# Performance work log

Measured on AMD Instinct MI355X. Metric: run time of the kernel, lower is better.

## Reference

```python
import jax, jax.numpy as jnp
import numpy as np

B, I, C, J, D, H, W = 16, 32, 8, 10, 16, 6, 6
NUM_ROUTING = 3
EPS = 1e-07


def setup_inputs() -> dict:
    key = jax.random.key(0)
    u_hat = jax.random.normal(key, (B, I, C, J, D, H, W), dtype=jnp.float32)
    # torch module fills bias with 0.1, shape (out_capsules, out_channels, 1, 1)
    bias = jnp.full((J, D, 1, 1), 0.1, dtype=jnp.float32)
    return {"u_hat": u_hat, "bias": bias, "num_routing": NUM_ROUTING}


def _squash(s):
    # Faithful to the source: L1 norm over ALL non-batch dims (not per-capsule L2).
    n1 = jnp.sum(jnp.abs(s), axis=(1, 2, 3, 4), keepdims=True)  # [B,1,1,1,1]
    n1_sq = n1 * n1
    return (n1_sq / (1.0 + n1_sq)) * (s / (n1 + EPS))


def reference(u_hat, bias, num_routing):
    # u_hat: [B,I,C,J,D,H,W]; bias: [J,D,1,1]
    b_ij = jnp.zeros((I, J), dtype=u_hat.dtype)
    v_j = None
    for _ in range(num_routing):
        c_ij = jax.nn.softmax(b_ij, axis=1)  # [I,J]
        # s_j[b,j,d,h,w] = sum_{i,c} c[i,j] * u_hat[b,i,c,j,d,h,w]  (c broadcast over in_channels)
        s_j = jnp.einsum('ij,bicjdhw->bjdhw', c_ij, u_hat) + bias
        v_j = _squash(s_j)  # [B,J,D,H,W]
        # agreement[i,j] = sum over b,c,d,h,w of u_hat * v_j (broadcast over i,c)
        agreement = jnp.einsum('bicjdhw,bjdhw->ij', u_hat, v_j)
        b_ij = b_ij + jax.lax.stop_gradient(agreement)  # torch uses .data (detached)
    return v_j
```

## Files before the change

kernel.cpp:

```cpp
#include <hip/hip_runtime.h>


#define NB   16
#define NI   32
#define NC   8
#define NJ   10
#define ND   16
#define NHW  36
#define NDHW 576
#define CK   3
#define CHK  192
#define NBJ  (NB * NJ)
#define NBJC (NBJ * CK)
#define NJDHW (NJ * NDHW)
#define NTOT  (NB * NJ * NDHW)
#define EPSV 1e-7f
#define TPB  192

static __device__ __forceinline__ double wave_sum(double v) {
    #pragma unroll
    for (int off = 32; off > 0; off >>= 1) v += __shfl_down(v, off);
    return v;
}

static __device__ __forceinline__ void n1_reduce(float sv, double* slot,
                                                 double* nred ) {
    int tid = threadIdx.x;
    double a = wave_sum((double)fabsf(sv));
    if ((tid & 63) == 0) nred[tid >> 6] = a;
    __syncthreads();
    if (tid == 0) slot[0] = (nred[0] + nred[1]) + nred[2];
}

static __device__ __forceinline__ void g_reduce(const float* Uv, float sv,
                                                double* gslot,
                                                double (*gred)[32] ) {
    int tid = threadIdx.x, w = tid >> 6, lane = tid & 63;
    #pragma unroll
    for (int i = 0; i < NI; ++i) {
        double p = wave_sum((double)Uv[i] * (double)sv);
        if (lane == 0) gred[w][i] = p;
    }
    __syncthreads();
    if (tid < NI)
        gslot[tid] = (gred[0][tid] + gred[1][tid]) + gred[2][tid];
}

__global__ __launch_bounds__(TPB) void a1_kernel(
    const float4* __restrict__ uh4, const float* __restrict__ bias,
    float4* __restrict__ U2f4, double* __restrict__ n1p, double* __restrict__ Gp)
{
    __shared__ float4  Utile4[NI * 48];
    __shared__ double  nred[3];
    __shared__ double  gred[3][32];

    const int blk = blockIdx.x;
    const int bj = blk / CK, ck = blk - bj * CK;
    const int b = bj / NJ,  j  = bj - b * NJ;
    const int tid = threadIdx.x;

    #pragma unroll
    for (int g = 0; g < 8; ++g) {
        int lin = g * TPB + tid;
        int i  = lin / 48, f4 = lin - i * 48;
        const float4* p = uh4 + ((size_t)(b * NI + i) * NC) * 1440
                              + j * 144 + ck * 48 + f4;
        float4 acc = make_float4(0.f, 0.f, 0.f, 0.f);
        #pragma unroll
        for (int c = 0; c < NC; ++c) {
            float4 v = p[(size_t)c * 1440];
            acc.x += v.x; acc.y += v.y; acc.z += v.z; acc.w += v.w;
        }
        Utile4[lin] = acc;
        U2f4[(size_t)bj * 4608 + i * 144 + ck * 48 + f4] = acc;
    }
    __syncthreads();

    const float* Utile = (const float*)Utile4;
    const float cw = 1.0f / 10.0f;
    float Uv[NI];
    float sv = bias[j * ND + (ck * CHK + tid) / NHW];
    #pragma unroll
    for (int i = 0; i < NI; ++i) {
        Uv[i] = Utile[i * CHK + tid];
        sv += cw * Uv[i];
    }

    n1_reduce(sv, &n1p[blk], nred);
    g_reduce(Uv, sv, &Gp[(size_t)blk * NI], gred);
}

template <int R>
__global__ __launch_bounds__(TPB) void ab_kernel(
    const float* __restrict__ U2, const float* __restrict__ bias,
    const double* __restrict__ n1p, double* __restrict__ Gp,
    double* __restrict__ n1p_out, double* __restrict__ Gp_out,
    float* __restrict__ s)
{
    __shared__ double sc_sh[2][NB];
    __shared__ float  bij_sh[NI * NJ];
    __shared__ float  c_sh[NI];
    __shared__ double nred[3];
    __shared__ double gred[3][32];

    const int blk = blockIdx.x;
    const int bj = blk / CK, ck = blk - bj * CK;
    const int b = bj / NJ,  j  = bj - b * NJ;
    const int tid = threadIdx.x;

    if (tid < R * NB) {
        int rr = tid / NB, bb = tid - rr * NB;
        double n1 = 0.0;
        #pragma unroll
        for (int jj = 0; jj < NJ; ++jj)
            #pragma unroll
            for (int cc = 0; cc < CK; ++cc)
                n1 += n1p[(size_t)rr * NBJC + (bb * NJ + jj) * CK + cc];
        double nsq = n1 * n1;
        sc_sh[rr][bb] = (nsq / (1.0 + nsq)) / (n1 + (double)EPSV);
    }
    __syncthreads();

    for (int e = tid; e < NI * NJ; e += TPB) {
        int i = e / NJ, jj = e - i * NJ;
        double a = 0.0;
        for (int rr = 0; rr < R; ++rr)
            #pragma unroll
            for (int bb = 0; bb < NB; ++bb)
                #pragma unroll
                for (int cc = 0; cc < CK; ++cc)
                    a += sc_sh[rr][bb] *
                         Gp[(size_t)rr * (NBJC * NI) +
                            (size_t)((bb * NJ + jj) * CK + cc) * NI + i];
        bij_sh[e] = (float)a;
    }
    __syncthreads();

    if (tid < NI) {
        float m = -1e30f;
        #pragma unroll
        for (int jj = 0; jj < NJ; ++jj) m = fmaxf(m, bij_sh[tid * NJ + jj]);
        float sum = 0.f;
        #pragma unroll
        for (int jj = 0; jj < NJ; ++jj) sum += expf(bij_sh[tid * NJ + jj] - m);
        c_sh[tid] = expf(bij_sh[tid * NJ + j] - m) / sum;
    }
    __syncthreads();

    const float* u2b = U2 + (size_t)bj * 18432 + ck * CHK + tid;
    float Uv[NI];
    float sv = bias[j * ND + (ck * CHK + tid) / NHW];
    #pragma unroll
    for (int i = 0; i < NI; ++i) {
        Uv[i] = u2b[i * NDHW];
        sv += c_sh[i] * Uv[i];
    }

    if (R == 2) s[(size_t)bj * NDHW + ck * CHK + tid] = sv;

    n1_reduce(sv, &n1p_out[blk], nred);
    if (R == 1)
        g_reduce(Uv, sv, &Gp_out[(size_t)blk * NI], gred);
}

__global__ __launch_bounds__(256) void v_kernel(
    const float* __restrict__ s, const double* __restrict__ n1p2,
    float* __restrict__ out)
{
    int e = blockIdx.x * 256 + threadIdx.x;
    int b = e / NJDHW;
    double n1 = 0.0;
    #pragma unroll
    for (int jj = 0; jj < NJ; ++jj)
        #pragma unroll
        for (int cc = 0; cc < CK; ++cc)
            n1 += n1p2[(b * NJ + jj) * CK + cc];
    float n1f = (float)n1;
    float nsq = n1f * n1f;
    out[e] = (nsq / (1.f + nsq)) * (s[e] / (n1f + EPSV));
}

extern "C" void kernel_launch(void* const* d_in, const int* in_sizes, int n_in,
                              void* d_out, int out_size, void* d_ws, size_t ws_size,
                              hipStream_t stream)
{
    const float* u_hat = (const float*)d_in[0];
    const float* bias  = (const float*)d_in[1];

    float*  U2  = (float*)d_ws;
    float*  s   = U2 + (size_t)NB * NJ * NI * NDHW;
    double* n1p = (double*)(s + NTOT);
    double* Gp  = n1p + 3 * NBJC;
    float*  out = (float*)d_out;

    a1_kernel<<<NBJC, TPB, 0, stream>>>(
        (const float4*)u_hat, bias, (float4*)U2, n1p, Gp);
    ab_kernel<1><<<NBJC, TPB, 0, stream>>>(
        U2, bias, n1p, Gp, n1p + NBJC, Gp + NBJC * NI, s);
    ab_kernel<2><<<NBJC, TPB, 0, stream>>>(
        U2, bias, n1p, Gp, n1p + 2 * NBJC, nullptr, s);
    v_kernel<<<NTOT / 256, 256, 0, stream>>>(s, n1p + 2 * NBJC, out);
}
```

Before: 209.3 us.

## Fuse final routing iteration and squash into per-batch kernel, transpose Gp layout

Replaces the second routing kernel and the separate squash kernel with one per-batch kernel. It computes all coupling coefficients, builds s in shared memory, reduces the L1 norm in-block and writes the output directly. This removes one launch and the global round trip of s. The partial-agreement buffer is also reordered so the b_ij reductions read contiguous memory. The trade-off is that the final kernel runs only 16 large blocks, which may underuse the GPU while streaming U2.

```diff
diff --git a/kernel.cpp b/kernel.cpp
--- a/kernel.cpp
+++ b/kernel.cpp
@@ -12,10 +12,15 @@
 #define CHK  192
 #define NBJ  (NB * NJ)
 #define NBJC (NBJ * CK)
-#define NJDHW (NJ * NDHW)
 #define NTOT  (NB * NJ * NDHW)
 #define EPSV 1e-7f
 #define TPB  192
+#define FTPB 1024
+#define GP_ITER (NJ * NI * NB * CK)
+#define GP_J    (NI * NB * CK)
+#define GP_I    (NB * CK)
+#define N1_ITER (NB * NJ * CK)
+#define N1_B    (NJ * CK)
 
 static __device__ __forceinline__ double wave_sum(double v) {
     #pragma unroll
@@ -32,9 +37,9 @@
     if (tid == 0) slot[0] = (nred[0] + nred[1]) + nred[2];
 }
 
-static __device__ __forceinline__ void g_reduce(const float* Uv, float sv,
-                                                double* gslot,
-                                                double (*gred)[32] ) {
+static __device__ __forceinline__ void g_reduce_t(const float* Uv, float sv,
+                                                  double* gbase,
+                                                  double (*gred)[32] ) {
     int tid = threadIdx.x, w = tid >> 6, lane = tid & 63;
     #pragma unroll
     for (int i = 0; i < NI; ++i) {
@@ -43,7 +48,7 @@
     }
     __syncthreads();
     if (tid < NI)
-        gslot[tid] = (gred[0][tid] + gred[1][tid]) + gred[2][tid];
+        gbase[tid * GP_I] = (gred[0][tid] + gred[1][tid]) + gred[2][tid];
 }
 
 __global__ __launch_bounds__(TPB) void a1_kernel(
@@ -86,18 +91,15 @@
         sv += cw * Uv[i];
     }
 
-    n1_reduce(sv, &n1p[blk], nred);
-    g_reduce(Uv, sv, &Gp[(size_t)blk * NI], gred);
-}
-
-template <int R>
-__global__ __launch_bounds__(TPB) void ab_kernel(
+    n1_reduce(sv, &n1p[b * N1_B + j * CK + ck], nred);
+    g_reduce_t(Uv, sv, Gp + j * GP_J + b * CK + ck, gred);
+}
+
+__global__ __launch_bounds__(TPB) void ab1_kernel(
     const float* __restrict__ U2, const float* __restrict__ bias,
-    const double* __restrict__ n1p, double* __restrict__ Gp,
-    double* __restrict__ n1p_out, double* __restrict__ Gp_out,
-    float* __restrict__ s)
-{
-    __shared__ double sc_sh[2][NB];
+    double* __restrict__ n1p, double* __restrict__ Gp)
+{
+    __shared__ double sc_sh[NB];
     __shared__ float  bij_sh[NI * NJ];
     __shared__ float  c_sh[NI];
     __shared__ double nred[3];
@@ -108,76 +110,147 @@
     const int b = bj / NJ,  j  = bj - b * NJ;
     const int tid = threadIdx.x;
 
-    if (tid < R * NB) {
+    if (tid < NB) {
+        const double* np = n1p + tid * N1_B;
+        double n1 = 0.0;
+        #pragma unroll
+        for (int jj = 0; jj < NJ; ++jj)
+            #pragma unroll
+            for (int cc = 0; cc < CK; ++cc) n1 += np[jj * CK + cc];
+        double nsq = n1 * n1;
+        sc_sh[tid] = (nsq / (1.0 + nsq)) / (n1 + (double)EPSV);
+    }
+    __syncthreads();
+
+    for (int e = tid; e < NI * NJ; e += TPB) {
+        int i = e / NJ, jj = e - i * NJ;
+        const double* g = Gp + jj * GP_J + i * GP_I;
+        double a = 0.0;
+        #pragma unroll
+        for (int bb = 0; bb < NB; ++bb)
+            #pragma unroll
+            for (int cc = 0; cc < CK; ++cc)
+                a += sc_sh[bb] * g[bb * CK + cc];
+        bij_sh[e] = (float)a;
+    }
+    __syncthreads();
+
+    if (tid < NI) {
+        float m = -1e30f;
+        #pragma unroll
+        for (int jj = 0; jj < NJ; ++jj) m = fmaxf(m, bij_sh[tid * NJ + jj]);
+        float sum = 0.f;
+        #pragma unroll
+        for (int jj = 0; jj < NJ; ++jj) sum += expf(bij_sh[tid * NJ + jj] - m);
+        c_sh[tid] = expf(bij_sh[tid * NJ + j] - m) / sum;
+    }
+    __syncthreads();
+
+    const float* u2b = U2 + (size_t)bj * 18432 + ck * CHK + tid;
+    float Uv[NI];
+    float sv = bias[j * ND + (ck * CHK + tid) / NHW];
+    #pragma unroll
+    for (int i = 0; i < NI; ++i) {
+        Uv[i] = u2b[i * NDHW];
+        sv += c_sh[i] * Uv[i];
+    }
+
+    n1_reduce(sv, &n1p[N1_ITER + b * N1_B + j * CK + ck], nred);
+    g_reduce_t(Uv, sv, Gp + GP_ITER + j * GP_J + b * CK + ck, gred);
+}
+
+__global__ __launch_bounds__(FTPB) void final_kernel(
+    const float* __restrict__ U2, const float* __restrict__ bias,
+    const double* __restrict__ n1p, const double* __restrict__ Gp,
+    float* __restrict__ out)
+{
+    __shared__ float  s_sh[NJ * NDHW];
+    __shared__ double gpart[90];
+    __shared__ double sc_sh[2][NB];
+    __shared__ float  bij_sh[NI * NJ];
+    __shared__ float  c_sh[NI * NJ];
+    __shared__ double n1_sh;
+
+    const int b = blockIdx.x;
+    const int tid = threadIdx.x;
+
+    if (tid < 2 * NB) {
         int rr = tid / NB, bb = tid - rr * NB;
+        const double* np = n1p + (size_t)rr * N1_ITER + bb * N1_B;
         double n1 = 0.0;
         #pragma unroll
         for (int jj = 0; jj < NJ; ++jj)
             #pragma unroll
-            for (int cc = 0; cc < CK; ++cc)
-                n1 += n1p[(size_t)rr * NBJC + (bb * NJ + jj) * CK + cc];
+            for (int cc = 0; cc < CK; ++cc) n1 += np[jj * CK + cc];
         double nsq = n1 * n1;
         sc_sh[rr][bb] = (nsq / (1.0 + nsq)) / (n1 + (double)EPSV);
     }
     __syncthreads();
 
-    for (int e = tid; e < NI * NJ; e += TPB) {
-        int i = e / NJ, jj = e - i * NJ;
+    if (tid < NI * NJ) {
+        int i = tid / NJ, jj = tid - i * NJ;
         double a = 0.0;
-        for (int rr = 0; rr < R; ++rr)
+        for (int rr = 0; rr < 2; ++rr) {
+            const double* g = Gp + (size_t)rr * GP_ITER + jj * GP_J + i * GP_I;
             #pragma unroll
             for (int bb = 0; bb < NB; ++bb)
                 #pragma unroll
                 for (int cc = 0; cc < CK; ++cc)
-                    a += sc_sh[rr][bb] *
-                         Gp[(size_t)rr * (NBJC * NI) +
-                            (size_t)((bb * NJ + jj) * CK + cc) * NI + i];
-        bij_sh[e] = (float)a;
-    }
-    __syncthreads();
-
-    if (tid < NI) {
+                    a += sc_sh[rr][bb] * g[bb * CK + cc];
+        }
+        bij_sh[tid] = (float)a;
+    }
+    __syncthreads();
+
+    if (tid < NI * NJ) {
+        int i = tid / NJ;
         float m = -1e30f;
         #pragma unroll
-        for (int jj = 0; jj < NJ; ++jj) m = fmaxf(m, bij_sh[tid * NJ + jj]);
+        for (int j2 = 0; j2 < NJ; ++j2) m = fmaxf(m, bij_sh[i * NJ + j2]);
         float sum = 0.f;
         #pragma unroll
-        for (int jj = 0; jj < NJ; ++jj) sum += expf(bij_sh[tid * NJ + jj] - m);
-        c_sh[tid] = expf(bij_sh[tid * NJ + j] - m) / sum;
-    }
-    __syncthreads();
-
-    const float* u2b = U2 + (size_t)bj * 18432 + ck * CHK + tid;
-    float Uv[NI];
-    float sv = bias[j * ND + (ck * CHK + tid) / NHW];
-    #pragma unroll
-    for (int i = 0; i < NI; ++i) {
-        Uv[i] = u2b[i * NDHW];
-        sv += c_sh[i] * Uv[i];
-    }
-
-    if (R == 2) s[(size_t)bj * NDHW + ck * CHK + tid] = sv;
-
-    n1_reduce(sv, &n1p_out[blk], nred);
-    if (R == 1)
-        g_reduce(Uv, sv, &Gp_out[(size_t)blk * NI], gred);
-}
-
-__global__ __launch_bounds__(256) void v_kernel(
-    const float* __restrict__ s, const double* __restrict__ n1p2,
-    float* __restrict__ out)
-{
-    int e = blockIdx.x * 256 + threadIdx.x;
-    int b = e / NJDHW;
-    double n1 = 0.0;
-    #pragma unroll
-    for (int jj = 0; jj < NJ; ++jj)
-        #pragma unroll
-        for (int cc = 0; cc < CK; ++cc)
-            n1 += n1p2[(b * NJ + jj) * CK + cc];
-    float n1f = (float)n1;
+        for (int j2 = 0; j2 < NJ; ++j2) sum += expf(bij_sh[i * NJ + j2] - m);
+        c_sh[tid] = expf(bij_sh[tid] - m) / sum;
+    }
+    __syncthreads();
+
+    const float* u2b0 = U2 + (size_t)b * (NJ * NI * NDHW);
+    for (int e = tid; e < NJ * NDHW; e += FTPB) {
+        int jj = e / NDHW, dhw = e - jj * NDHW;
+        const float* up = u2b0 + jj * (NI * NDHW) + dhw;
+        float sv = bias[jj * ND + dhw / NHW];
+        #pragma unroll
+        for (int i = 0; i < NI; ++i) sv += c_sh[i * NJ + jj] * up[i * NDHW];
+        s_sh[e] = sv;
+    }
+    __syncthreads();
+
+    {
+        int wv = tid >> 6, lane = tid & 63;
+        for (int g = wv; g < 90; g += (FTPB / 64)) {
+            double a = wave_sum((double)fabsf(s_sh[g * 64 + lane]));
+            if (lane == 0) gpart[g] = a;
+        }
+    }
+    __syncthreads();
+    if (tid == 0) {
+        double n1 = 0.0;
+        #pragma unroll
+        for (int jj = 0; jj < NJ; ++jj)
+            #pragma unroll
+            for (int cc = 0; cc < CK; ++cc) {
+                int gg = jj * 9 + cc * 3;
+                n1 += (gpart[gg] + gpart[gg + 1]) + gpart[gg + 2];
+            }
+        n1_sh = n1;
+    }
+    __syncthreads();
+
+    float n1f = (float)n1_sh;
     float nsq = n1f * n1f;
-    out[e] = (nsq / (1.f + nsq)) * (s[e] / (n1f + EPSV));
+    float* ob = out + (size_t)b * (NJ * NDHW);
+    for (int e = tid; e < NJ * NDHW; e += FTPB)
+        ob[e] = (nsq / (1.f + nsq)) * (s_sh[e] / (n1f + EPSV));
 }
 
 extern "C" void kernel_launch(void* const* d_in, const int* in_sizes, int n_in,
@@ -186,18 +259,14 @@
 {
     const float* u_hat = (const float*)d_in[0];
     const float* bias  = (const float*)d_in[1];
+    float* out = (float*)d_out;
 
     float*  U2  = (float*)d_ws;
-    float*  s   = U2 + (size_t)NB * NJ * NI * NDHW;
-    double* n1p = (double*)(s + NTOT);
-    double* Gp  = n1p + 3 * NBJC;
-    float*  out = (float*)d_out;
+    double* n1p = (double*)(U2 + (size_t)NB * NJ * NI * NDHW);
+    double* Gp  = n1p + 2 * N1_ITER;
 
     a1_kernel<<<NBJC, TPB, 0, stream>>>(
         (const float4*)u_hat, bias, (float4*)U2, n1p, Gp);
-    ab_kernel<1><<<NBJC, TPB, 0, stream>>>(
-        U2, bias, n1p, Gp, n1p + NBJC, Gp + NBJC * NI, s);
-    ab_kernel<2><<<NBJC, TPB, 0, stream>>>(
-        U2, bias, n1p, Gp, n1p + 2 * NBJC, nullptr, s);
-    v_kernel<<<NTOT / 256, 256, 0, stream>>>(s, n1p + 2 * NBJC, out);
-}
+    ab1_kernel<<<NBJC, TPB, 0, stream>>>(U2, bias, n1p, Gp);
+    final_kernel<<<NB, FTPB, 0, stream>>>(U2, bias, n1p, Gp, out);
+}
```

Result: faster. 192.7 us (-7.9%).
